# Kernel tuning notes

Measured on AMD Instinct MI355X. Metric: run time of the kernel, lower is better.

## Reference

```python
import jax, jax.numpy as jnp
import numpy as np
import math

B, M, N, K = 4, 8192, 8192, 16
FD = 64       # in_fdim == out_fdim (residual add)
HID = 128     # args.hidden_dim
G = 8         # args.ngroups


def index_points(points, idx):
    # points: (B, C, N), idx: (B, M, K) -> (B, C, M, K)
    return jax.vmap(lambda p, i: p[:, i])(points, idx)


def conv1d(x, w, b):  # 1x1 Conv1d: x (B,Ci,M), w (Co,Ci)
    return jnp.einsum('oi,bim->bom', w, x) + b[None, :, None]


def conv2d(x, w, b):  # 1x1 Conv2d: x (B,Ci,M,K), w (Co,Ci)
    return jnp.einsum('oi,bimk->bomk', w, x) + b[None, :, None, None]


def group_norm(x, w, b, eps=1e-5):
    # torch GroupNorm over (C//G, M, K) per group per sample
    Bb, C, Mm, Kk = x.shape
    xr = x.reshape(Bb, G, C // G, Mm, Kk)
    mu = xr.mean(axis=(2, 3, 4), keepdims=True)
    var = xr.var(axis=(2, 3, 4), keepdims=True)
    xr = (xr - mu) * jax.lax.rsqrt(var + eps)
    return xr.reshape(Bb, C, Mm, Kk) * w[None, :, None, None] + b[None, :, None, None]


def setup_inputs() -> dict:
    key = jax.random.key(0)
    ks = jax.random.split(key, 24)
    s = 0.05
    inp = {
        'q_xyzs': jax.random.normal(ks[0], (B, 3, M), jnp.float32),
        'k_xyzs': jax.random.normal(ks[1], (B, 3, N), jnp.float32),
        'q_feats': jax.random.normal(ks[2], (B, FD, M), jnp.float32),
        'k_feats': jax.random.normal(ks[3], (B, FD, N), jnp.float32),
        'v_feats': jax.random.normal(ks[4], (B, FD, N), jnp.float32),
        'knn_idx': jax.random.randint(ks[5], (B, M, K), 0, N),
        'mask': jnp.ones((B, M, K), dtype=bool),
        'wq_w': jax.random.normal(ks[6], (HID, FD)) * s, 'wq_b': jnp.zeros((HID,)),
        'wk_w': jax.random.normal(ks[7], (HID, FD)) * s, 'wk_b': jnp.zeros((HID,)),
        'wv_w': jax.random.normal(ks[8], (HID, FD)) * s, 'wv_b': jnp.zeros((HID,)),
        'd1_w': jax.random.normal(ks[9], (HID, 3)) * s, 'd1_b': jnp.zeros((HID,)),
        'dgn_w': jnp.ones((HID,)), 'dgn_b': jnp.zeros((HID,)),
        'd2_w': jax.random.normal(ks[10], (HID, HID)) * s, 'd2_b': jnp.zeros((HID,)),
        'g1_w': jax.random.normal(ks[11], (HID, HID)) * s, 'g1_b': jnp.zeros((HID,)),
        'ggn_w': jnp.ones((HID,)), 'ggn_b': jnp.zeros((HID,)),
        'g2_w': jax.random.normal(ks[12], (HID, HID)) * s, 'g2_b': jnp.zeros((HID,)),
        'post_w': jax.random.normal(ks[13], (FD, HID)) * s, 'post_b': jnp.zeros((FD,)),
    }
    return inp


def reference(q_xyzs, k_xyzs, q_feats, k_feats, v_feats, knn_idx, mask,
              wq_w, wq_b, wk_w, wk_b, wv_w, wv_b,
              d1_w, d1_b, dgn_w, dgn_b, d2_w, d2_b,
              g1_w, g1_b, ggn_w, ggn_b, g2_w, g2_b,
              post_w, post_b):
    knn_xyzs = index_points(k_xyzs, knn_idx)                 # (B,3,M,K)
    pre = q_feats
    query = conv1d(q_feats, wq_w, wq_b)                      # (B,HID,M)
    key = index_points(conv1d(k_feats, wk_w, wk_b), knn_idx) # (B,HID,M,K)
    value = index_points(conv1d(v_feats, wv_w, wv_b), knn_idx)

    rel = q_xyzs[:, :, :, None] - knn_xyzs                   # (B,3,M,K)
    pos_enc = conv2d(jax.nn.relu(group_norm(conv2d(rel, d1_w, d1_b), dgn_w, dgn_b)), d2_w, d2_b)

    attn_in = query[:, :, :, None] - key + pos_enc
    attn = conv2d(jax.nn.relu(group_norm(conv2d(attn_in, g1_w, g1_b), ggn_w, ggn_b)), g2_w, g2_b)
    attn = attn / math.sqrt(HID)
    attn = jnp.where(mask[:, None], attn, -jnp.finfo(attn.dtype).max)
    attn = jax.nn.softmax(attn, axis=-1)                     # over neighbor axis K

    res = jnp.einsum('bcmk,bcmk->bcm', attn, value + pos_enc)
    return conv1d(res, post_w, post_b) + pre
```

## Files before the change

### kernel.cpp

```cpp
#include <hip/hip_runtime.h>
#include <hip/hip_bf16.h>

typedef __attribute__((ext_vector_type(8))) short short8;
typedef __attribute__((ext_vector_type(4))) float f32x4;
typedef unsigned short ushort_t;

#define B_    4
#define M_    8192
#define N_    8192
#define KNN   16
#define FD    64
#define HID   128
#define CNT   (M_*KNN)
#define SCALE 0.08838834764831845f

#define QT_OFF       0ULL
#define KT_OFF       4194304ULL
#define VT_OFF       6291456ULL
#define WD2_OFF      8388608ULL
#define WFO_OFF      8396800ULL
#define WG2_OFF      8404992ULL
#define WQ2T_OFF     8413184ULL
#define WK2T_OFF     8421376ULL
#define WVT_OFF      8429568ULL
#define POSTT_OFF    8437760ULL
#define G2BS_OFF     8445952ULL
#define BQ_OFF       8446080ULL
#define BK_OFF       8446208ULL
#define HAFF_OFF     8446336ULL
#define RELSTATS_OFF 8448384ULL
#define YSUM_OFF     8448448ULL
#define YSQ_OFF      8448960ULL
#define GGNA_OFF     8449472ULL
#define GGNB_OFF     8449984ULL

__device__ __forceinline__ ushort_t f2bf(float x) {
    return (ushort_t)((__float_as_uint(x) + 0x8000u) >> 16);
}
__device__ __forceinline__ unsigned pk2bf(float a, float b) {
    unsigned ua = __float_as_uint(a) + 0x8000u;
    unsigned ub = __float_as_uint(b) + 0x8000u;
    return (ua >> 16) | (ub & 0xFFFF0000u);
}
__device__ __forceinline__ float bf2f(ushort_t b) {
    union { unsigned u; float f; } v; v.u = ((unsigned)b) << 16;
    return v.f;
}

__global__ __launch_bounds__(256) void k_prep(
    const float* __restrict__ d2, const float* __restrict__ g1, const float* __restrict__ g2,
    const float* __restrict__ wq, const float* __restrict__ wk, const float* __restrict__ wv,
    const float* __restrict__ post, const float* __restrict__ g2b,
    const float* __restrict__ wq_b, const float* __restrict__ wk_b,
    const float* __restrict__ d2b, const float* __restrict__ g1b,
    float* __restrict__ ws)
{
    int tid = blockIdx.x * 256 + threadIdx.x;
    if (tid < 16384) {
        int j = tid & 7, lane = (tid >> 3) & 63, s = (tid >> 9) & 3, ct = tid >> 11;
        int row = ct*16 + (lane & 15);
        int colk = s*32 + (lane >> 4)*8 + j;
        ((ushort_t*)(ws + WD2_OFF))[tid] = f2bf(d2[row*HID + colk]);
        ((ushort_t*)(ws + WG2_OFF))[tid] = f2bf(g2[row*HID + colk] * SCALE);
        float acc = 0.f;
        #pragma unroll 8
        for (int t = 0; t < HID; t++) acc += g1[row*HID + t] * d2[t*HID + colk];
        ((ushort_t*)(ws + WFO_OFF))[tid] = f2bf(acc);
    }
    if (tid < 8192) {
        int f = tid >> 7, j = tid & 127;
        ws[POSTT_OFF + j*64 + f] = post[tid];
        int i = tid >> 7, c = tid & 127;
        float aq = 0.f, ak = 0.f;
        #pragma unroll 8
        for (int h = 0; h < HID; h++) {
            float g = g1[c*HID + h];
            aq += g * wq[h*FD + i];
            ak += g * wk[h*FD + i];
        }
        ws[WQ2T_OFF + tid] = aq;
        ws[WK2T_OFF + tid] = ak;
        ws[WVT_OFF + tid] = wv[c*FD + i];
    }
    if (tid < 128) {
        ws[G2BS_OFF + tid] = g2b[tid] * SCALE;
        float bq = g1b[tid], bk = 0.f;
        #pragma unroll 8
        for (int h = 0; h < HID; h++) {
            float g = g1[tid*HID + h];
            bq += g * (wq_b[h] + d2b[h]);
            bk += g * wk_b[h];
        }
        ws[BQ_OFF + tid] = bq;
        ws[BK_OFF + tid] = bk;
    }
}

__global__ __launch_bounds__(256) void k_transform(
    const float* __restrict__ qf, const float* __restrict__ kf, const float* __restrict__ vf,
    const float* __restrict__ wv_b, float* __restrict__ ws)
{
    __shared__ __align__(16) float sF[64*36];
    int tid = threadIdx.x;
    int t = blockIdx.y;
    int gm0 = blockIdx.x * 32;
    int b = gm0 >> 13, m0 = gm0 & (M_-1);
    const float* in = (t==0) ? qf : (t==1) ? kf : vf;
    const float* wT = ws + ((t==0) ? WQ2T_OFF : (t==1) ? WK2T_OFF : WVT_OFF);
    {
        int i = tid >> 2, sg = tid & 3;
        const float* src = in + ((size_t)b*FD + i)*M_ + m0 + sg*8;
        *(f32x4*)&sF[i*36 + sg*8]     = *(const f32x4*)src;
        *(f32x4*)&sF[i*36 + sg*8 + 4] = *(const f32x4*)(src + 4);
    }
    __syncthreads();
    int c = tid & 127, h = tid >> 7;
    float bc = (t==0) ? ws[BQ_OFF + c] : (t==1) ? ws[BK_OFF + c] : wv_b[c];
    float acc[16];
    #pragma unroll
    for (int p = 0; p < 16; p++) acc[p] = bc;
    #pragma unroll 4
    for (int i = 0; i < 64; i++) {
        float w = wT[i*128 + c];
        #pragma unroll
        for (int pq = 0; pq < 4; pq++) {
            f32x4 fv = *(const f32x4*)&sF[i*36 + h*16 + pq*4];
            acc[pq*4+0] += w*fv[0]; acc[pq*4+1] += w*fv[1];
            acc[pq*4+2] += w*fv[2]; acc[pq*4+3] += w*fv[3];
        }
    }
    if (t == 0) {
        #pragma unroll
        for (int p = 0; p < 16; p++)
            ws[QT_OFF + (size_t)(gm0 + h*16 + p)*HID + c] = acc[p];
    } else {
        ushort_t* o = (ushort_t*)(ws + ((t==1) ? KT_OFF : VT_OFF));
        #pragma unroll
        for (int p = 0; p < 16; p++)
            o[(size_t)(gm0 + h*16 + p)*HID + c] = f2bf(acc[p]);
    }
}

__global__ __launch_bounds__(256) void k_relstats(
    const float* __restrict__ qx, const float* __restrict__ kx,
    const int* __restrict__ knn, float* __restrict__ ws)
{
    int tid = threadIdx.x;
    int b = blockIdx.y;
    int m = blockIdx.x * 256 + tid;
    const float* qb = qx + (size_t)b*3*M_;
    const float* kb = kx + (size_t)b*3*N_;
    const int* kn = knn + ((size_t)b*M_ + m)*KNN;
    float a[9] = {0,0,0,0,0,0,0,0,0};
    float q0 = qb[m], q1 = qb[M_+m], q2 = qb[2*M_+m];
    #pragma unroll
    for (int k = 0; k < KNN; k++) {
        int id = kn[k];
        float r0 = q0 - kb[id], r1 = q1 - kb[N_+id], r2 = q2 - kb[2*N_+id];
        a[0]+=r0; a[1]+=r1; a[2]+=r2;
        a[3]+=r0*r0; a[4]+=r0*r1; a[5]+=r0*r2;
        a[6]+=r1*r1; a[7]+=r1*r2; a[8]+=r2*r2;
    }
    __shared__ float red[4];
    float* rs = ws + RELSTATS_OFF + b*16;
    for (int q = 0; q < 9; q++) {
        float v = a[q];
        #pragma unroll
        for (int o = 32; o > 0; o >>= 1) v += __shfl_down(v, o, 64);
        if ((tid & 63) == 0) red[tid >> 6] = v;
        __syncthreads();
        if (tid == 0) atomicAdd(&rs[q], red[0]+red[1]+red[2]+red[3]);
        __syncthreads();
    }
}

__global__ __launch_bounds__(512) void k_dgn(
    const float* __restrict__ d1w, const float* __restrict__ d1b,
    const float* __restrict__ gw, const float* __restrict__ gb,
    float* __restrict__ ws)
{
    __shared__ float sm_[512], sq_[512], smu[32], srs[32];
    int t = threadIdx.x, b = t >> 7, c = t & 127;
    const float* rs = ws + RELSTATS_OFF + b*16;
    float inv = 1.0f / (float)CNT;
    float x0 = rs[0]*inv, x1 = rs[1]*inv, x2 = rs[2]*inv;
    float S00 = rs[3]*inv, S01 = rs[4]*inv, S02 = rs[5]*inv;
    float S11 = rs[6]*inv, S12 = rs[7]*inv, S22 = rs[8]*inv;
    float w0 = d1w[c*3], w1 = d1w[c*3+1], w2 = d1w[c*3+2], bc = d1b[c];
    float mc = w0*x0 + w1*x1 + w2*x2 + bc;
    float qc = w0*w0*S00 + w1*w1*S11 + w2*w2*S22
             + 2.f*(w0*w1*S01 + w0*w2*S02 + w1*w2*S12)
             + 2.f*bc*(mc - bc) + bc*bc;
    sm_[t] = mc; sq_[t] = qc;
    __syncthreads();
    if (t < 32) {
        int bb = t >> 3, g = t & 7;
        float mu = 0, ey = 0;
        for (int j = 0; j < 16; j++) { mu += sm_[bb*128 + g*16 + j]; ey += sq_[bb*128 + g*16 + j]; }
        mu *= (1.f/16.f); ey *= (1.f/16.f);
        smu[t] = mu; srs[t] = rsqrtf(ey - mu*mu + 1e-5f);
    }
    __syncthreads();
    int g = c >> 4;
    float al = gw[c] * srs[b*8 + g];
    float be = gb[c] - smu[b*8 + g] * al;
    f32x4 h; h[0] = al*w0; h[1] = al*w1; h[2] = al*w2; h[3] = al*bc + be;
    *(f32x4*)(ws + HAFF_OFF + ((size_t)b*128 + c)*4) = h;
}

__global__ __launch_bounds__(512) void k_ggn(
    const float* __restrict__ gw, const float* __restrict__ gb, float* __restrict__ ws)
{
    __shared__ float smu[32], srs[32];
    int t = threadIdx.x, b = t >> 7, c = t & 127;
    if (t < 32) {
        int bb = t >> 3, g = t & 7;
        float s1 = 0, s2 = 0;
        for (int j = 0; j < 16; j++) {
            s1 += ws[YSUM_OFF + bb*128 + g*16 + j];
            s2 += ws[YSQ_OFF  + bb*128 + g*16 + j];
        }
        float invn = 1.f / (16.f * (float)CNT);
        float mu = s1*invn, ey = s2*invn;
        smu[t] = mu; srs[t] = rsqrtf(ey - mu*mu + 1e-5f);
    }
    __syncthreads();
    int g = c >> 4;
    float al = gw[c] * srs[b*8 + g];
    float be = gb[c] - smu[b*8 + g] * al;
    ws[GGNA_OFF + b*128 + c] = al;
    ws[GGNB_OFF + b*128 + c] = be;
}

struct SmemPipe {
    union {
        ushort_t tP[4][16*136];
        struct { f32x4 haff[128]; float rel[4][16][4]; } pre;
    } u;
    ushort_t tH[4][16*136];
    float ga[128], gb[128];
    float res[4][128];
    int idx[64];
};

template<bool STATS>
__global__ __launch_bounds__(256, 4) void k_pipe(
    const float* __restrict__ qx, const float* __restrict__ kx, const int* __restrict__ knn,
    const float* __restrict__ qf, const float* __restrict__ d2b, const float* __restrict__ postb,
    float* __restrict__ ws, float* __restrict__ out)
{
    __shared__ SmemPipe sm;
    int tid = threadIdx.x, wid = tid >> 6, lane = tid & 63;
    int ln = lane & 15, q = lane >> 4;
    int gm0 = blockIdx.x * 4;
    int b = gm0 >> 13, m0 = gm0 & (M_-1);
    int ct0 = wid * 2;

    if (tid < 64) {
        int id = knn[(size_t)gm0*KNN + tid];
        sm.idx[tid] = id;
        int p = tid >> 4, nn = tid & 15;
        int m = m0 + p;
        sm.u.pre.rel[p][nn][0] = qx[(size_t)b*3*M_ + m]        - kx[(size_t)b*3*N_ + id];
        sm.u.pre.rel[p][nn][1] = qx[(size_t)b*3*M_ + M_ + m]   - kx[(size_t)b*3*N_ + N_ + id];
        sm.u.pre.rel[p][nn][2] = qx[(size_t)b*3*M_ + 2*M_ + m] - kx[(size_t)b*3*N_ + 2*N_ + id];
    }
    if (tid < 128) {
        sm.u.pre.haff[tid] = *(const f32x4*)(ws + HAFF_OFF + ((size_t)b*128 + tid)*4);
        if (STATS) { sm.ga[tid] = 0.f; sm.gb[tid] = 0.f; }
        else { sm.ga[tid] = ws[GGNA_OFF + b*128 + tid]; sm.gb[tid] = ws[GGNB_OFF + b*128 + tid]; }
    }
    __syncthreads();

    {
        int p = tid >> 6, n = (tid >> 2) & 15, cb = tid & 3;
        float r0 = sm.u.pre.rel[p][n][0];
        float r1 = sm.u.pre.rel[p][n][1];
        float r2 = sm.u.pre.rel[p][n][2];
        unsigned* dst = (unsigned*)&sm.tH[p][n*136 + cb*32];
        #pragma unroll
        for (int jj = 0; jj < 32; jj += 2) {
            f32x4 h1 = sm.u.pre.haff[cb*32 + jj];
            f32x4 h2 = sm.u.pre.haff[cb*32 + jj + 1];
            float a = fmaf(h1[0], r0, fmaf(h1[1], r1, fmaf(h1[2], r2, h1[3])));
            float c = fmaf(h2[0], r0, fmaf(h2[1], r1, fmaf(h2[2], r2, h2[3])));
            dst[jj >> 1] = pk2bf(a > 0.f ? a : 0.f, c > 0.f ? c : 0.f);
        }
    }
    __syncthreads();

    const short8* wd2 = (const short8*)(ws + WD2_OFF);
    const short8* wfo = (const short8*)(ws + WFO_OFF);
    const ushort_t* ktb = (const ushort_t*)(ws + KT_OFF);
    const ushort_t* vtb = (const ushort_t*)(ws + VT_OFF);

    f32x4 bid2[2], gav[2], gbv[2];
    if (!STATS) {
        #pragma unroll
        for (int cc = 0; cc < 2; cc++) {
            int row0 = (ct0+cc)*16 + q*4;
            bid2[cc] = *(const f32x4*)(d2b + row0);
            gav[cc] = *(const f32x4*)&sm.ga[row0];
            gbv[cc] = *(const f32x4*)&sm.gb[row0];
        }
    }
    float s1[2][4], s2[2][4];
    if (STATS) {
        #pragma unroll
        for (int cc = 0; cc < 2; cc++)
            #pragma unroll
            for (int r = 0; r < 4; r++) { s1[cc][r] = 0.f; s2[cc][r] = 0.f; }
    }

    for (int p = 0; p < 4; p++) {
        int gm = gm0 + p;
        short8 bh[4];
        #pragma unroll
        for (int s = 0; s < 4; s++)
            bh[s] = *(const short8*)&sm.tH[p][ln*136 + s*32 + q*8];

        f32x4 accY[2];
        #pragma unroll
        for (int cc = 0; cc < 2; cc++) {
            f32x4 a = {0.f,0.f,0.f,0.f};
            #pragma unroll
            for (int s = 0; s < 4; s++)
                a = __builtin_amdgcn_mfma_f32_16x16x32_bf16(wfo[((ct0+cc)*4+s)*64 + lane], bh[s], a, 0,0,0);
            accY[cc] = a;
        }
        if (!STATS) {
            #pragma unroll
            for (int cc = 0; cc < 2; cc++) {
                f32x4 a = {0.f,0.f,0.f,0.f};
                #pragma unroll
                for (int s = 0; s < 4; s++)
                    a = __builtin_amdgcn_mfma_f32_16x16x32_bf16(wd2[((ct0+cc)*4+s)*64 + lane], bh[s], a, 0,0,0);
                int row0 = (ct0+cc)*16 + q*4;
                uint2 pv;
                pv.x = pk2bf(a[0]+bid2[cc][0], a[1]+bid2[cc][1]);
                pv.y = pk2bf(a[2]+bid2[cc][2], a[3]+bid2[cc][3]);
                *(uint2*)&sm.u.tP[p][ln*136 + row0] = pv;
            }
        }
        int id = sm.idx[p*16 + ln];
        float yv[2][4];
        #pragma unroll
        for (int cc = 0; cc < 2; cc++) {
            int row0 = (ct0+cc)*16 + q*4;
            f32x4 qv = *(const f32x4*)(ws + QT_OFF + (size_t)gm*HID + row0);
            uint2 kv = *(const uint2*)(ktb + ((size_t)b*N_ + id)*HID + row0);
            yv[cc][0] = accY[cc][0] + qv[0] - bf2f((ushort_t)(kv.x & 0xffff));
            yv[cc][1] = accY[cc][1] + qv[1] - bf2f((ushort_t)(kv.x >> 16));
            yv[cc][2] = accY[cc][2] + qv[2] - bf2f((ushort_t)(kv.y & 0xffff));
            yv[cc][3] = accY[cc][3] + qv[3] - bf2f((ushort_t)(kv.y >> 16));
        }
        if (STATS) {
            #pragma unroll
            for (int cc = 0; cc < 2; cc++)
                #pragma unroll
                for (int r = 0; r < 4; r++) { s1[cc][r] += yv[cc][r]; s2[cc][r] += yv[cc][r]*yv[cc][r]; }
        } else {
            __syncthreads();
            #pragma unroll
            for (int cc = 0; cc < 2; cc++) {
                int row0 = (ct0+cc)*16 + q*4;
                float y0 = fmaf(gav[cc][0], yv[cc][0], gbv[cc][0]);
                float y1 = fmaf(gav[cc][1], yv[cc][1], gbv[cc][1]);
                float y2 = fmaf(gav[cc][2], yv[cc][2], gbv[cc][2]);
                float y3 = fmaf(gav[cc][3], yv[cc][3], gbv[cc][3]);
                uint2 yw;
                yw.x = pk2bf(y0 > 0.f ? y0 : 0.f, y1 > 0.f ? y1 : 0.f);
                yw.y = pk2bf(y2 > 0.f ? y2 : 0.f, y3 > 0.f ? y3 : 0.f);
                *(uint2*)&sm.tH[p][ln*136 + row0] = yw;
            }
        }
    }

    if (STATS) {
        #pragma unroll
        for (int cc = 0; cc < 2; cc++)
            #pragma unroll
            for (int r = 0; r < 4; r++) {
                float v1 = s1[cc][r], v2 = s2[cc][r];
                v1 += __shfl_xor(v1,1,64); v1 += __shfl_xor(v1,2,64);
                v1 += __shfl_xor(v1,4,64); v1 += __shfl_xor(v1,8,64);
                v2 += __shfl_xor(v2,1,64); v2 += __shfl_xor(v2,2,64);
                v2 += __shfl_xor(v2,4,64); v2 += __shfl_xor(v2,8,64);
                if (ln == 0) {
                    atomicAdd(&sm.ga[(ct0+cc)*16 + q*4 + r], v1);
                    atomicAdd(&sm.gb[(ct0+cc)*16 + q*4 + r], v2);
                }
            }
        __syncthreads();
        if (tid < 128) {
            atomicAdd(&ws[YSUM_OFF + b*128 + tid], sm.ga[tid]);
            atomicAdd(&ws[YSQ_OFF  + b*128 + tid], sm.gb[tid]);
        }
        return;
    }

    {
        int p = tid >> 6, n = (tid >> 2) & 15, cb = tid & 3;
        int id = sm.idx[p*16 + n];
        const ushort_t* vr = vtb + ((size_t)b*N_ + id)*HID + cb*32;
        ushort_t* pr = &sm.u.tP[p][n*136 + cb*32];
        #pragma unroll
        for (int u = 0; u < 4; u++) {
            short8 vv = *(const short8*)(vr + u*8);
            short8 pp = *(const short8*)(pr + u*8);
            unsigned w[4];
            #pragma unroll
            for (int j = 0; j < 4; j++) {
                float a = bf2f((ushort_t)vv[j*2])   + bf2f((ushort_t)pp[j*2]);
                float c = bf2f((ushort_t)vv[j*2+1]) + bf2f((ushort_t)pp[j*2+1]);
                w[j] = pk2bf(a, c);
            }
            *(short8*)(pr + u*8) = *(short8*)w;
        }
    }
    __syncthreads();

    {
        const short8* wg2 = (const short8*)(ws + WG2_OFF);
        #pragma unroll
        for (int p = 0; p < 4; p++) {
            short8 ay[4];
            #pragma unroll
            for (int s = 0; s < 4; s++)
                ay[s] = *(const short8*)&sm.tH[p][ln*136 + s*32 + q*8];
            #pragma unroll
            for (int cc = 0; cc < 2; cc++) {
                int cout = (ct0+cc)*16 + ln;
                f32x4 a = {0.f,0.f,0.f,0.f};
                #pragma unroll
                for (int s = 0; s < 4; s++)
                    a = __builtin_amdgcn_mfma_f32_16x16x32_bf16(ay[s], wg2[((ct0+cc)*4+s)*64 + lane], a, 0,0,0);
                float zb = ws[G2BS_OFF + cout];
                float den = 0.f, num = 0.f;
                #pragma unroll
                for (int r = 0; r < 4; r++) {
                    float e = __expf(a[r] + zb);
                    den += e;
                    num += e * bf2f(sm.u.tP[p][(q*4+r)*136 + cout]);
                }
                den += __shfl_xor(den, 16, 64); den += __shfl_xor(den, 32, 64);
                num += __shfl_xor(num, 16, 64); num += __shfl_xor(num, 32, 64);
                if (q == 0) sm.res[p][cout] = num / den;
            }
        }
    }
    __syncthreads();

    {
        int f = tid >> 2, p = tid & 3;
        const float* pt = ws + POSTT_OFF;
        const float* rr = sm.res[p];
        float acc = postb[f];
        #pragma unroll 8
        for (int j = 0; j < 128; j++) acc += pt[j*64 + f] * rr[j];
        size_t o = (size_t)b*FD*M_ + (size_t)f*M_ + m0 + p;
        out[o] = acc + qf[o];
    }
}

extern "C" void kernel_launch(void* const* d_in, const int* in_sizes, int n_in,
                              void* d_out, int out_size, void* d_ws, size_t ws_size,
                              hipStream_t stream)
{
    const float* q_xyzs = (const float*)d_in[0];
    const float* k_xyzs = (const float*)d_in[1];
    const float* q_feats= (const float*)d_in[2];
    const float* k_feats= (const float*)d_in[3];
    const float* v_feats= (const float*)d_in[4];
    const int*   knn    = (const int*)d_in[5];
    const float* wq_w = (const float*)d_in[7];  const float* wq_b = (const float*)d_in[8];
    const float* wk_w = (const float*)d_in[9];  const float* wk_b = (const float*)d_in[10];
    const float* wv_w = (const float*)d_in[11]; const float* wv_b = (const float*)d_in[12];
    const float* d1_w = (const float*)d_in[13]; const float* d1_b = (const float*)d_in[14];
    const float* dgn_w= (const float*)d_in[15]; const float* dgn_b= (const float*)d_in[16];
    const float* d2_w = (const float*)d_in[17]; const float* d2_b = (const float*)d_in[18];
    const float* g1_w = (const float*)d_in[19]; const float* g1_b = (const float*)d_in[20];
    const float* ggn_w= (const float*)d_in[21]; const float* ggn_b= (const float*)d_in[22];
    const float* g2_w = (const float*)d_in[23]; const float* g2_b = (const float*)d_in[24];
    const float* post_w=(const float*)d_in[25]; const float* post_b=(const float*)d_in[26];
    float* ws  = (float*)d_ws;
    float* out = (float*)d_out;

    hipMemsetAsync(ws + RELSTATS_OFF, 0, 1088*sizeof(float), stream);

    k_prep<<<64, 256, 0, stream>>>(d2_w, g1_w, g2_w, wq_w, wk_w, wv_w,
                                   post_w, g2_b, wq_b, wk_b, d2_b, g1_b, ws);
    k_transform<<<dim3(B_*M_/32, 3), 256, 0, stream>>>(q_feats, k_feats, v_feats, wv_b, ws);
    k_relstats<<<dim3(M_/256, B_), 256, 0, stream>>>(q_xyzs, k_xyzs, knn, ws);
    k_dgn<<<1, 512, 0, stream>>>(d1_w, d1_b, dgn_w, dgn_b, ws);
    k_pipe<true><<<B_*M_/4, 256, 0, stream>>>(
        q_xyzs, k_xyzs, knn, q_feats, d2_b, post_b, ws, out);
    k_ggn<<<1, 512, 0, stream>>>(ggn_w, ggn_b, ws);
    k_pipe<false><<<B_*M_/4, 256, 0, stream>>>(
        q_xyzs, k_xyzs, knn, q_feats, d2_b, post_b, ws, out);
}
```

Before: 527.0 us.

## Cache pre-norm attention activations between passes and stage output through transpose kernel

The stats pass now writes the pre-GroupNorm activations to the workspace as bf16 when enough workspace is available. The second pass reloads them instead of recomputing the first MFMA product and the key gather. Key gathers are issued early to hide latency, and the rel-projection loop is rotated to reduce LDS bank conflicts. The final output is staged in the workspace and transposed by a new k_out kernel for coalesced stores. This trades extra HBM traffic (about 64MB written and read) for less recompute and gather work, plus one extra launch.

```diff
diff --git a/kernel.cpp b/kernel.cpp
--- a/kernel.cpp
+++ b/kernel.cpp
@@ -33,6 +33,9 @@
 #define YSQ_OFF      8448960ULL
 #define GGNA_OFF     8449472ULL
 #define GGNB_OFF     8449984ULL
+#define OUTS_OFF     8450496ULL
+#define YW_OFF       10547648ULL
+#define WS_NEED_BIG  ((10547648ULL + 16777216ULL) * 4ULL)
 
 __device__ __forceinline__ ushort_t f2bf(float x) {
     return (ushort_t)((__float_as_uint(x) + 0x8000u) >> 16);
@@ -243,11 +246,11 @@
     int idx[64];
 };
 
-template<bool STATS>
+template<bool STATS, bool STOREY, bool LOADY>
 __global__ __launch_bounds__(256, 4) void k_pipe(
     const float* __restrict__ qx, const float* __restrict__ kx, const int* __restrict__ knn,
-    const float* __restrict__ qf, const float* __restrict__ d2b, const float* __restrict__ postb,
-    float* __restrict__ ws, float* __restrict__ out)
+    const float* __restrict__ d2b, const float* __restrict__ postb,
+    float* __restrict__ ws)
 {
     __shared__ SmemPipe sm;
     int tid = threadIdx.x, wid = tid >> 6, lane = tid & 63;
@@ -272,38 +275,43 @@
     }
     __syncthreads();
 
+    const ushort_t* ktb = (const ushort_t*)(ws + KT_OFF);
+    const ushort_t* vtb = (const ushort_t*)(ws + VT_OFF);
+
+    uint2 kvp[4][2];
+    if (!LOADY) {
+        #pragma unroll
+        for (int p = 0; p < 4; p++) {
+            int id = sm.idx[p*16 + ln];
+            const ushort_t* kr = ktb + ((size_t)b*N_ + id)*HID;
+            #pragma unroll
+            for (int cc = 0; cc < 2; cc++)
+                kvp[p][cc] = *(const uint2*)(kr + (ct0+cc)*16 + q*4);
+        }
+    }
+
     {
         int p = tid >> 6, n = (tid >> 2) & 15, cb = tid & 3;
         float r0 = sm.u.pre.rel[p][n][0];
         float r1 = sm.u.pre.rel[p][n][1];
         float r2 = sm.u.pre.rel[p][n][2];
         unsigned* dst = (unsigned*)&sm.tH[p][n*136 + cb*32];
-        #pragma unroll
-        for (int jj = 0; jj < 32; jj += 2) {
-            f32x4 h1 = sm.u.pre.haff[cb*32 + jj];
-            f32x4 h2 = sm.u.pre.haff[cb*32 + jj + 1];
+        int rot = ((((n >> 3) & 1) | (((cb >> 1) & 1) << 1)) << 2);
+        #pragma unroll
+        for (int t = 0; t < 16; t++) {
+            int o = (t + rot) & 15;
+            f32x4 h1 = sm.u.pre.haff[cb*32 + 2*o];
+            f32x4 h2 = sm.u.pre.haff[cb*32 + 2*o + 1];
             float a = fmaf(h1[0], r0, fmaf(h1[1], r1, fmaf(h1[2], r2, h1[3])));
             float c = fmaf(h2[0], r0, fmaf(h2[1], r1, fmaf(h2[2], r2, h2[3])));
-            dst[jj >> 1] = pk2bf(a > 0.f ? a : 0.f, c > 0.f ? c : 0.f);
-        }
-    }
-    __syncthreads();
-
+            dst[o] = pk2bf(a > 0.f ? a : 0.f, c > 0.f ? c : 0.f);
+        }
+    }
+    __syncthreads();
+
+    const short8* wfo = (const short8*)(ws + WFO_OFF);
     const short8* wd2 = (const short8*)(ws + WD2_OFF);
-    const short8* wfo = (const short8*)(ws + WFO_OFF);
-    const ushort_t* ktb = (const ushort_t*)(ws + KT_OFF);
-    const ushort_t* vtb = (const ushort_t*)(ws + VT_OFF);
-
-    f32x4 bid2[2], gav[2], gbv[2];
-    if (!STATS) {
-        #pragma unroll
-        for (int cc = 0; cc < 2; cc++) {
-            int row0 = (ct0+cc)*16 + q*4;
-            bid2[cc] = *(const f32x4*)(d2b + row0);
-            gav[cc] = *(const f32x4*)&sm.ga[row0];
-            gbv[cc] = *(const f32x4*)&sm.gb[row0];
-        }
-    }
+
     float s1[2][4], s2[2][4];
     if (STATS) {
         #pragma unroll
@@ -311,7 +319,19 @@
             #pragma unroll
             for (int r = 0; r < 4; r++) { s1[cc][r] = 0.f; s2[cc][r] = 0.f; }
     }
-
+    uint2 yp[4][2];
+    f32x4 bid2[2], ga_[2], gb_[2];
+    #pragma unroll
+    for (int cc = 0; cc < 2; cc++) {
+        int row0 = (ct0+cc)*16 + q*4;
+        if (!STATS) {
+            bid2[cc] = *(const f32x4*)(d2b + row0);
+            ga_[cc] = *(const f32x4*)&sm.ga[row0];
+            gb_[cc] = *(const f32x4*)&sm.gb[row0];
+        }
+    }
+
+    #pragma unroll
     for (int p = 0; p < 4; p++) {
         int gm = gm0 + p;
         short8 bh[4];
@@ -319,14 +339,33 @@
         for (int s = 0; s < 4; s++)
             bh[s] = *(const short8*)&sm.tH[p][ln*136 + s*32 + q*8];
 
-        f32x4 accY[2];
-        #pragma unroll
-        for (int cc = 0; cc < 2; cc++) {
-            f32x4 a = {0.f,0.f,0.f,0.f};
-            #pragma unroll
-            for (int s = 0; s < 4; s++)
-                a = __builtin_amdgcn_mfma_f32_16x16x32_bf16(wfo[((ct0+cc)*4+s)*64 + lane], bh[s], a, 0,0,0);
-            accY[cc] = a;
+        if (!LOADY) {
+            #pragma unroll
+            for (int cc = 0; cc < 2; cc++) {
+                int row0 = (ct0+cc)*16 + q*4;
+                f32x4 a = {0.f,0.f,0.f,0.f};
+                #pragma unroll
+                for (int s = 0; s < 4; s++)
+                    a = __builtin_amdgcn_mfma_f32_16x16x32_bf16(wfo[((ct0+cc)*4+s)*64 + lane], bh[s], a, 0,0,0);
+                f32x4 qv = *(const f32x4*)(ws + QT_OFF + (size_t)gm*HID + row0);
+                uint2 kv = kvp[p][cc];
+                float y0 = a[0] + qv[0] - bf2f((ushort_t)(kv.x & 0xffff));
+                float y1 = a[1] + qv[1] - bf2f((ushort_t)(kv.x >> 16));
+                float y2 = a[2] + qv[2] - bf2f((ushort_t)(kv.y & 0xffff));
+                float y3 = a[3] + qv[3] - bf2f((ushort_t)(kv.y >> 16));
+                if (STATS) {
+                    s1[cc][0]+=y0; s1[cc][1]+=y1; s1[cc][2]+=y2; s1[cc][3]+=y3;
+                    s2[cc][0]+=y0*y0; s2[cc][1]+=y1*y1; s2[cc][2]+=y2*y2; s2[cc][3]+=y3*y3;
+                    if (STOREY) { yp[p][cc].x = pk2bf(y0,y1); yp[p][cc].y = pk2bf(y2,y3); }
+                } else {
+                    float t0 = fmaf(ga_[cc][0], y0, gb_[cc][0]);
+                    float t1 = fmaf(ga_[cc][1], y1, gb_[cc][1]);
+                    float t2 = fmaf(ga_[cc][2], y2, gb_[cc][2]);
+                    float t3 = fmaf(ga_[cc][3], y3, gb_[cc][3]);
+                    yp[p][cc].x = pk2bf(t0 > 0.f ? t0 : 0.f, t1 > 0.f ? t1 : 0.f);
+                    yp[p][cc].y = pk2bf(t2 > 0.f ? t2 : 0.f, t3 > 0.f ? t3 : 0.f);
+                }
+            }
         }
         if (!STATS) {
             #pragma unroll
@@ -342,41 +381,26 @@
                 *(uint2*)&sm.u.tP[p][ln*136 + row0] = pv;
             }
         }
-        int id = sm.idx[p*16 + ln];
-        float yv[2][4];
-        #pragma unroll
-        for (int cc = 0; cc < 2; cc++) {
-            int row0 = (ct0+cc)*16 + q*4;
-            f32x4 qv = *(const f32x4*)(ws + QT_OFF + (size_t)gm*HID + row0);
-            uint2 kv = *(const uint2*)(ktb + ((size_t)b*N_ + id)*HID + row0);
-            yv[cc][0] = accY[cc][0] + qv[0] - bf2f((ushort_t)(kv.x & 0xffff));
-            yv[cc][1] = accY[cc][1] + qv[1] - bf2f((ushort_t)(kv.x >> 16));
-            yv[cc][2] = accY[cc][2] + qv[2] - bf2f((ushort_t)(kv.y & 0xffff));
-            yv[cc][3] = accY[cc][3] + qv[3] - bf2f((ushort_t)(kv.y >> 16));
-        }
-        if (STATS) {
-            #pragma unroll
-            for (int cc = 0; cc < 2; cc++)
+    }
+
+    if (STATS) {
+        if (STOREY) {
+            __syncthreads();
+            #pragma unroll
+            for (int p = 0; p < 4; p++)
                 #pragma unroll
-                for (int r = 0; r < 4; r++) { s1[cc][r] += yv[cc][r]; s2[cc][r] += yv[cc][r]*yv[cc][r]; }
-        } else {
+                for (int cc = 0; cc < 2; cc++)
+                    *(uint2*)&sm.tH[p][ln*136 + (ct0+cc)*16 + q*4] = yp[p][cc];
             __syncthreads();
-            #pragma unroll
-            for (int cc = 0; cc < 2; cc++) {
-                int row0 = (ct0+cc)*16 + q*4;
-                float y0 = fmaf(gav[cc][0], yv[cc][0], gbv[cc][0]);
-                float y1 = fmaf(gav[cc][1], yv[cc][1], gbv[cc][1]);
-                float y2 = fmaf(gav[cc][2], yv[cc][2], gbv[cc][2]);
-                float y3 = fmaf(gav[cc][3], yv[cc][3], gbv[cc][3]);
-                uint2 yw;
-                yw.x = pk2bf(y0 > 0.f ? y0 : 0.f, y1 > 0.f ? y1 : 0.f);
-                yw.y = pk2bf(y2 > 0.f ? y2 : 0.f, y3 > 0.f ? y3 : 0.f);
-                *(uint2*)&sm.tH[p][ln*136 + row0] = yw;
-            }
-        }
-    }
-
-    if (STATS) {
+            {
+                int p = tid >> 6, n = (tid >> 2) & 15, cb = tid & 3;
+                ushort_t* yw = (ushort_t*)(ws + YW_OFF);
+                const short8* src = (const short8*)&sm.tH[p][n*136 + cb*32];
+                short8* dst = (short8*)(yw + ((size_t)(gm0+p)*16 + n)*HID + cb*32);
+                #pragma unroll
+                for (int u = 0; u < 4; u++) dst[u] = src[u];
+            }
+        }
         #pragma unroll
         for (int cc = 0; cc < 2; cc++)
             #pragma unroll
@@ -399,6 +423,36 @@
         return;
     }
 
+    __syncthreads();
+
+    if (LOADY) {
+        int p = tid >> 6, n = (tid >> 2) & 15, cb = tid & 3;
+        const ushort_t* yw = (const ushort_t*)(ws + YW_OFF);
+        const short8* src = (const short8*)(yw + ((size_t)(gm0+p)*16 + n)*HID + cb*32);
+        ushort_t* dst = &sm.tH[p][n*136 + cb*32];
+        #pragma unroll
+        for (int u = 0; u < 4; u++) {
+            short8 yv8 = src[u];
+            f32x4 a0 = *(const f32x4*)&sm.ga[cb*32 + u*8];
+            f32x4 a1 = *(const f32x4*)&sm.ga[cb*32 + u*8 + 4];
+            f32x4 b0 = *(const f32x4*)&sm.gb[cb*32 + u*8];
+            f32x4 b1 = *(const f32x4*)&sm.gb[cb*32 + u*8 + 4];
+            unsigned w[4];
+            #pragma unroll
+            for (int j = 0; j < 4; j++) {
+                float ya = fmaf((j<2?a0:a1)[(j*2)&3],   bf2f((ushort_t)yv8[j*2]),   (j<2?b0:b1)[(j*2)&3]);
+                float yb = fmaf((j<2?a0:a1)[(j*2+1)&3], bf2f((ushort_t)yv8[j*2+1]), (j<2?b0:b1)[(j*2+1)&3]);
+                w[j] = pk2bf(ya > 0.f ? ya : 0.f, yb > 0.f ? yb : 0.f);
+            }
+            *(short8*)(dst + u*8) = *(short8*)w;
+        }
+    } else {
+        #pragma unroll
+        for (int p = 0; p < 4; p++)
+            #pragma unroll
+            for (int cc = 0; cc < 2; cc++)
+                *(uint2*)&sm.tH[p][ln*136 + (ct0+cc)*16 + q*4] = yp[p][cc];
+    }
     {
         int p = tid >> 6, n = (tid >> 2) & 15, cb = tid & 3;
         int id = sm.idx[p*16 + n];
@@ -458,8 +512,29 @@
         float acc = postb[f];
         #pragma unroll 8
         for (int j = 0; j < 128; j++) acc += pt[j*64 + f] * rr[j];
-        size_t o = (size_t)b*FD*M_ + (size_t)f*M_ + m0 + p;
-        out[o] = acc + qf[o];
+        ws[OUTS_OFF + (size_t)(gm0 + p)*FD + f] = acc;
+    }
+}
+
+__global__ __launch_bounds__(256) void k_out(
+    const float* __restrict__ qf, const float* __restrict__ ws, float* __restrict__ out)
+{
+    __shared__ float sT[64][65];
+    int tid = threadIdx.x;
+    int b = blockIdx.y, m0 = blockIdx.x * 64;
+    const float* stg = ws + OUTS_OFF + ((size_t)b*M_ + m0)*FD;
+    #pragma unroll
+    for (int it = 0; it < 16; it++) {
+        int idx = it*256 + tid;
+        sT[idx >> 6][idx & 63] = stg[idx];
+    }
+    __syncthreads();
+    #pragma unroll
+    for (int it = 0; it < 16; it++) {
+        int idx = it*256 + tid;
+        int f = idx >> 6, mm = idx & 63;
+        size_t o = (size_t)b*FD*M_ + (size_t)f*M_ + m0 + mm;
+        out[o] = sT[mm][f] + qf[o];
     }
 }
 
@@ -486,6 +561,8 @@
     float* ws  = (float*)d_ws;
     float* out = (float*)d_out;
 
+    bool big = (ws_size >= WS_NEED_BIG);
+
     hipMemsetAsync(ws + RELSTATS_OFF, 0, 1088*sizeof(float), stream);
 
     k_prep<<<64, 256, 0, stream>>>(d2_w, g1_w, g2_w, wq_w, wk_w, wv_w,
@@ -493,9 +570,14 @@
     k_transform<<<dim3(B_*M_/32, 3), 256, 0, stream>>>(q_feats, k_feats, v_feats, wv_b, ws);
     k_relstats<<<dim3(M_/256, B_), 256, 0, stream>>>(q_xyzs, k_xyzs, knn, ws);
     k_dgn<<<1, 512, 0, stream>>>(d1_w, d1_b, dgn_w, dgn_b, ws);
-    k_pipe<true><<<B_*M_/4, 256, 0, stream>>>(
-        q_xyzs, k_xyzs, knn, q_feats, d2_b, post_b, ws, out);
+    if (big)
+        k_pipe<true, true, false><<<B_*M_/4, 256, 0, stream>>>(q_xyzs, k_xyzs, knn, d2_b, post_b, ws);
+    else
+        k_pipe<true, false, false><<<B_*M_/4, 256, 0, stream>>>(q_xyzs, k_xyzs, knn, d2_b, post_b, ws);
     k_ggn<<<1, 512, 0, stream>>>(ggn_w, ggn_b, ws);
-    k_pipe<false><<<B_*M_/4, 256, 0, stream>>>(
-        q_xyzs, k_xyzs, knn, q_feats, d2_b, post_b, ws, out);
-}
+    if (big)
+        k_pipe<false, false, true><<<B_*M_/4, 256, 0, stream>>>(q_xyzs, k_xyzs, knn, d2_b, post_b, ws);
+    else
+        k_pipe<false, false, false><<<B_*M_/4, 256, 0, stream>>>(q_xyzs, k_xyzs, knn, d2_b, post_b, ws);
+    k_out<<<dim3(M_/64, B_), 256, 0, stream>>>(q_feats, ws, out);
+}
```

Measured after the change: 488.4 us. 7.3% less time.

## Materialize pre-norm attention activations in stats pass and reuse in main pass

Applied to the files above, without the earlier changes.

The stats pass now writes the pre-GroupNorm attention activations (bf16, fragment layout) to workspace, and the main pass reloads them instead of recomputing the fused MFMA and re-gathering key rows. Key xyz coordinates are repacked into a float4-per-point table so each neighbour gather is one vector load. The query projection is stored as bf16, and the haff loop is rotated per thread to spread LDS bank access. The trade is an extra 64 MB write and read of intermediates in exchange for fewer gathers and MFMAs in the main kernel.

```diff
diff --git a/kernel.cpp b/kernel.cpp
--- a/kernel.cpp
+++ b/kernel.cpp
@@ -15,24 +15,27 @@
 #define SCALE 0.08838834764831845f
 
 #define QT_OFF       0ULL
-#define KT_OFF       4194304ULL
-#define VT_OFF       6291456ULL
-#define WD2_OFF      8388608ULL
-#define WFO_OFF      8396800ULL
-#define WG2_OFF      8404992ULL
-#define WQ2T_OFF     8413184ULL
-#define WK2T_OFF     8421376ULL
-#define WVT_OFF      8429568ULL
-#define POSTT_OFF    8437760ULL
-#define G2BS_OFF     8445952ULL
-#define BQ_OFF       8446080ULL
-#define BK_OFF       8446208ULL
-#define HAFF_OFF     8446336ULL
-#define RELSTATS_OFF 8448384ULL
-#define YSUM_OFF     8448448ULL
-#define YSQ_OFF      8448960ULL
-#define GGNA_OFF     8449472ULL
-#define GGNB_OFF     8449984ULL
+#define KT_OFF       2097152ULL
+#define VT_OFF       4194304ULL
+#define WD2_OFF      6291456ULL
+#define WFO_OFF      6299648ULL
+#define WG2_OFF      6307840ULL
+#define WQ2T_OFF     6316032ULL
+#define WK2T_OFF     6324224ULL
+#define WVT_OFF      6332416ULL
+#define POSTT_OFF    6340608ULL
+#define G2BS_OFF     6348800ULL
+#define BQ_OFF       6348928ULL
+#define BK_OFF       6349056ULL
+#define HAFF_OFF     6349184ULL
+#define RELSTATS_OFF 6351232ULL
+#define YSUM_OFF     6351296ULL
+#define YSQ_OFF      6351808ULL
+#define GGNA_OFF     6352320ULL
+#define GGNB_OFF     6352832ULL
+#define KXI_OFF      6353344ULL
+#define YW_OFF       6484416ULL
+#define WS_NEED_YW   ((YW_OFF + 33554432ULL) * 4ULL)
 
 __device__ __forceinline__ ushort_t f2bf(float x) {
     return (ushort_t)((__float_as_uint(x) + 0x8000u) >> 16);
@@ -53,7 +56,7 @@
     const float* __restrict__ post, const float* __restrict__ g2b,
     const float* __restrict__ wq_b, const float* __restrict__ wk_b,
     const float* __restrict__ d2b, const float* __restrict__ g1b,
-    float* __restrict__ ws)
+    const float* __restrict__ kx, float* __restrict__ ws)
 {
     int tid = blockIdx.x * 256 + threadIdx.x;
     if (tid < 16384) {
@@ -82,6 +85,19 @@
         ws[WK2T_OFF + tid] = ak;
         ws[WVT_OFF + tid] = wv[c*FD + i];
     }
+    #pragma unroll
+    for (int r = 0; r < 2; r++) {
+        int i = tid*2 + r;
+        if (i < B_*N_) {
+            int bb = i >> 13, id = i & (N_-1);
+            f32x4 v;
+            v[0] = kx[(size_t)bb*3*N_ + id];
+            v[1] = kx[(size_t)bb*3*N_ + N_ + id];
+            v[2] = kx[(size_t)bb*3*N_ + 2*N_ + id];
+            v[3] = 0.f;
+            *(f32x4*)(ws + KXI_OFF + (size_t)i*4) = v;
+        }
+    }
     if (tid < 128) {
         ws[G2BS_OFF + tid] = g2b[tid] * SCALE;
         float bq = g1b[tid], bk = 0.f;
@@ -129,34 +145,27 @@
             acc[pq*4+2] += w*fv[2]; acc[pq*4+3] += w*fv[3];
         }
     }
-    if (t == 0) {
-        #pragma unroll
-        for (int p = 0; p < 16; p++)
-            ws[QT_OFF + (size_t)(gm0 + h*16 + p)*HID + c] = acc[p];
-    } else {
-        ushort_t* o = (ushort_t*)(ws + ((t==1) ? KT_OFF : VT_OFF));
-        #pragma unroll
-        for (int p = 0; p < 16; p++)
-            o[(size_t)(gm0 + h*16 + p)*HID + c] = f2bf(acc[p]);
-    }
+    ushort_t* o = (ushort_t*)(ws + ((t==0) ? QT_OFF : (t==1) ? KT_OFF : VT_OFF));
+    #pragma unroll
+    for (int p = 0; p < 16; p++)
+        o[(size_t)(gm0 + h*16 + p)*HID + c] = f2bf(acc[p]);
 }
 
 __global__ __launch_bounds__(256) void k_relstats(
-    const float* __restrict__ qx, const float* __restrict__ kx,
-    const int* __restrict__ knn, float* __restrict__ ws)
+    const float* __restrict__ qx, const int* __restrict__ knn, float* __restrict__ ws)
 {
     int tid = threadIdx.x;
     int b = blockIdx.y;
     int m = blockIdx.x * 256 + tid;
     const float* qb = qx + (size_t)b*3*M_;
-    const float* kb = kx + (size_t)b*3*N_;
+    const f32x4* kxi = (const f32x4*)(ws + KXI_OFF) + (size_t)b*N_;
     const int* kn = knn + ((size_t)b*M_ + m)*KNN;
     float a[9] = {0,0,0,0,0,0,0,0,0};
     float q0 = qb[m], q1 = qb[M_+m], q2 = qb[2*M_+m];
     #pragma unroll
     for (int k = 0; k < KNN; k++) {
-        int id = kn[k];
-        float r0 = q0 - kb[id], r1 = q1 - kb[N_+id], r2 = q2 - kb[2*N_+id];
+        f32x4 kc = kxi[kn[k]];
+        float r0 = q0 - kc[0], r1 = q1 - kc[1], r2 = q2 - kc[2];
         a[0]+=r0; a[1]+=r1; a[2]+=r2;
         a[3]+=r0*r0; a[4]+=r0*r1; a[5]+=r0*r2;
         a[6]+=r1*r1; a[7]+=r1*r2; a[8]+=r2*r2;
@@ -232,7 +241,128 @@
     ws[GGNB_OFF + b*128 + c] = be;
 }
 
-struct SmemPipe {
+struct SmemS {
+    f32x4 haff[128];
+    float rel[4][16][4];
+    int idx[64];
+    ushort_t tH[4][16*136];
+    ushort_t tK[4][16*136];
+    float ga[128], gb[128];
+};
+
+__global__ __launch_bounds__(256, 4) void k_stats(
+    const float* __restrict__ qx, const int* __restrict__ knn, float* __restrict__ ws)
+{
+    __shared__ SmemS sm;
+    int tid = threadIdx.x, wid = tid >> 6, lane = tid & 63;
+    int ln = lane & 15, q = lane >> 4;
+    int gm0 = blockIdx.x * 4;
+    int b = gm0 >> 13, m0 = gm0 & (M_-1);
+    int ct0 = wid * 2;
+
+    if (tid < 64) {
+        int id = knn[(size_t)gm0*KNN + tid];
+        sm.idx[tid] = id;
+        int p = tid >> 4, nn = tid & 15;
+        int m = m0 + p;
+        f32x4 kc = *(const f32x4*)(ws + KXI_OFF + ((size_t)b*N_ + id)*4);
+        sm.rel[p][nn][0] = qx[(size_t)b*3*M_ + m]        - kc[0];
+        sm.rel[p][nn][1] = qx[(size_t)b*3*M_ + M_ + m]   - kc[1];
+        sm.rel[p][nn][2] = qx[(size_t)b*3*M_ + 2*M_ + m] - kc[2];
+    }
+    if (tid < 128) {
+        sm.haff[tid] = *(const f32x4*)(ws + HAFF_OFF + ((size_t)b*128 + tid)*4);
+        sm.ga[tid] = 0.f; sm.gb[tid] = 0.f;
+    }
+    __syncthreads();
+
+    const ushort_t* qtb = (const ushort_t*)(ws + QT_OFF);
+    const ushort_t* ktb = (const ushort_t*)(ws + KT_OFF);
+
+    {
+        int p = tid >> 6, n = (tid >> 2) & 15, cb = tid & 3;
+        int id = sm.idx[p*16 + n];
+        const short8* kr = (const short8*)(ktb + ((size_t)b*N_ + id)*HID + cb*32);
+        short8 kld0 = kr[0], kld1 = kr[1], kld2 = kr[2], kld3 = kr[3];
+
+        float r0 = sm.rel[p][n][0];
+        float r1 = sm.rel[p][n][1];
+        float r2 = sm.rel[p][n][2];
+        unsigned* dst = (unsigned*)&sm.tH[p][n*136 + cb*32];
+        int rot = ((((n >> 3) & 1) | (((cb >> 1) & 1) << 1)) << 2);
+        #pragma unroll
+        for (int t = 0; t < 16; t++) {
+            int o = (t + rot) & 15;
+            f32x4 h1 = sm.haff[cb*32 + 2*o];
+            f32x4 h2 = sm.haff[cb*32 + 2*o + 1];
+            float a = fmaf(h1[0], r0, fmaf(h1[1], r1, fmaf(h1[2], r2, h1[3])));
+            float c = fmaf(h2[0], r0, fmaf(h2[1], r1, fmaf(h2[2], r2, h2[3])));
+            dst[o] = pk2bf(a > 0.f ? a : 0.f, c > 0.f ? c : 0.f);
+        }
+        short8* kdst = (short8*)&sm.tK[p][n*136 + cb*32];
+        kdst[0] = kld0; kdst[1] = kld1; kdst[2] = kld2; kdst[3] = kld3;
+    }
+    __syncthreads();
+
+    const short8* wfo = (const short8*)(ws + WFO_OFF);
+    uint2* yw8 = (uint2*)(ws + YW_OFF);
+
+    float s1[2][4], s2[2][4];
+    #pragma unroll
+    for (int cc = 0; cc < 2; cc++)
+        #pragma unroll
+        for (int r = 0; r < 4; r++) { s1[cc][r] = 0.f; s2[cc][r] = 0.f; }
+
+    #pragma unroll
+    for (int p = 0; p < 4; p++) {
+        int gm = gm0 + p;
+        short8 bh[4];
+        #pragma unroll
+        for (int s = 0; s < 4; s++)
+            bh[s] = *(const short8*)&sm.tH[p][ln*136 + s*32 + q*8];
+
+        #pragma unroll
+        for (int cc = 0; cc < 2; cc++) {
+            f32x4 a = {0.f,0.f,0.f,0.f};
+            #pragma unroll
+            for (int s = 0; s < 4; s++)
+                a = __builtin_amdgcn_mfma_f32_16x16x32_bf16(wfo[((ct0+cc)*4+s)*64 + lane], bh[s], a, 0,0,0);
+            int row0 = (ct0+cc)*16 + q*4;
+            uint2 qv = *(const uint2*)(qtb + (size_t)gm*HID + row0);
+            uint2 kv = *(const uint2*)&sm.tK[p][ln*136 + row0];
+            float y0 = a[0] + bf2f((ushort_t)(qv.x & 0xffff)) - bf2f((ushort_t)(kv.x & 0xffff));
+            float y1 = a[1] + bf2f((ushort_t)(qv.x >> 16))    - bf2f((ushort_t)(kv.x >> 16));
+            float y2 = a[2] + bf2f((ushort_t)(qv.y & 0xffff)) - bf2f((ushort_t)(kv.y & 0xffff));
+            float y3 = a[3] + bf2f((ushort_t)(qv.y >> 16))    - bf2f((ushort_t)(kv.y >> 16));
+            s1[cc][0]+=y0; s1[cc][1]+=y1; s1[cc][2]+=y2; s1[cc][3]+=y3;
+            s2[cc][0]+=y0*y0; s2[cc][1]+=y1*y1; s2[cc][2]+=y2*y2; s2[cc][3]+=y3*y3;
+            uint2 yv; yv.x = pk2bf(y0,y1); yv.y = pk2bf(y2,y3);
+            yw8[((size_t)gm*8 + ct0+cc)*64 + lane] = yv;
+        }
+    }
+
+    #pragma unroll
+    for (int cc = 0; cc < 2; cc++)
+        #pragma unroll
+        for (int r = 0; r < 4; r++) {
+            float v1 = s1[cc][r], v2 = s2[cc][r];
+            v1 += __shfl_xor(v1,1,64); v1 += __shfl_xor(v1,2,64);
+            v1 += __shfl_xor(v1,4,64); v1 += __shfl_xor(v1,8,64);
+            v2 += __shfl_xor(v2,1,64); v2 += __shfl_xor(v2,2,64);
+            v2 += __shfl_xor(v2,4,64); v2 += __shfl_xor(v2,8,64);
+            if (ln == 0) {
+                atomicAdd(&sm.ga[(ct0+cc)*16 + q*4 + r], v1);
+                atomicAdd(&sm.gb[(ct0+cc)*16 + q*4 + r], v2);
+            }
+        }
+    __syncthreads();
+    if (tid < 128) {
+        atomicAdd(&ws[YSUM_OFF + b*128 + tid], sm.ga[tid]);
+        atomicAdd(&ws[YSQ_OFF  + b*128 + tid], sm.gb[tid]);
+    }
+}
+
+struct SmemM {
     union {
         ushort_t tP[4][16*136];
         struct { f32x4 haff[128]; float rel[4][16][4]; } pre;
@@ -243,34 +373,46 @@
     int idx[64];
 };
 
-template<bool STATS>
-__global__ __launch_bounds__(256, 4) void k_pipe(
-    const float* __restrict__ qx, const float* __restrict__ kx, const int* __restrict__ knn,
-    const float* __restrict__ qf, const float* __restrict__ d2b, const float* __restrict__ postb,
-    float* __restrict__ ws, float* __restrict__ out)
-{
-    __shared__ SmemPipe sm;
+__global__ __launch_bounds__(256, 4) void k_main(
+    const float* __restrict__ qx, const int* __restrict__ knn,
+    const float* __restrict__ d2b, const float* __restrict__ postb,
+    const float* __restrict__ qf, float* __restrict__ ws, float* __restrict__ out)
+{
+    __shared__ SmemM sm;
     int tid = threadIdx.x, wid = tid >> 6, lane = tid & 63;
     int ln = lane & 15, q = lane >> 4;
     int gm0 = blockIdx.x * 4;
     int b = gm0 >> 13, m0 = gm0 & (M_-1);
     int ct0 = wid * 2;
 
+    uint2 ywp[4][2];
+    {
+        const uint2* yw8 = (const uint2*)(ws + YW_OFF);
+        #pragma unroll
+        for (int p = 0; p < 4; p++)
+            #pragma unroll
+            for (int cc = 0; cc < 2; cc++)
+                ywp[p][cc] = yw8[((size_t)(gm0+p)*8 + ct0+cc)*64 + lane];
+    }
+
     if (tid < 64) {
         int id = knn[(size_t)gm0*KNN + tid];
         sm.idx[tid] = id;
         int p = tid >> 4, nn = tid & 15;
         int m = m0 + p;
-        sm.u.pre.rel[p][nn][0] = qx[(size_t)b*3*M_ + m]        - kx[(size_t)b*3*N_ + id];
-        sm.u.pre.rel[p][nn][1] = qx[(size_t)b*3*M_ + M_ + m]   - kx[(size_t)b*3*N_ + N_ + id];
-        sm.u.pre.rel[p][nn][2] = qx[(size_t)b*3*M_ + 2*M_ + m] - kx[(size_t)b*3*N_ + 2*N_ + id];
+        f32x4 kc = *(const f32x4*)(ws + KXI_OFF + ((size_t)b*N_ + id)*4);
+        sm.u.pre.rel[p][nn][0] = qx[(size_t)b*3*M_ + m]        - kc[0];
+        sm.u.pre.rel[p][nn][1] = qx[(size_t)b*3*M_ + M_ + m]   - kc[1];
+        sm.u.pre.rel[p][nn][2] = qx[(size_t)b*3*M_ + 2*M_ + m] - kc[2];
     }
     if (tid < 128) {
         sm.u.pre.haff[tid] = *(const f32x4*)(ws + HAFF_OFF + ((size_t)b*128 + tid)*4);
-        if (STATS) { sm.ga[tid] = 0.f; sm.gb[tid] = 0.f; }
-        else { sm.ga[tid] = ws[GGNA_OFF + b*128 + tid]; sm.gb[tid] = ws[GGNB_OFF + b*128 + tid]; }
-    }
-    __syncthreads();
+        sm.ga[tid] = ws[GGNA_OFF + b*128 + tid];
+        sm.gb[tid] = ws[GGNB_OFF + b*128 + tid];
+    }
+    __syncthreads();
+
+    const ushort_t* vtb = (const ushort_t*)(ws + VT_OFF);
 
     {
         int p = tid >> 6, n = (tid >> 2) & 15, cb = tid & 3;
@@ -278,127 +420,65 @@
         float r1 = sm.u.pre.rel[p][n][1];
         float r2 = sm.u.pre.rel[p][n][2];
         unsigned* dst = (unsigned*)&sm.tH[p][n*136 + cb*32];
-        #pragma unroll
-        for (int jj = 0; jj < 32; jj += 2) {
-            f32x4 h1 = sm.u.pre.haff[cb*32 + jj];
-            f32x4 h2 = sm.u.pre.haff[cb*32 + jj + 1];
+        int rot = ((((n >> 3) & 1) | (((cb >> 1) & 1) << 1)) << 2);
+        #pragma unroll
+        for (int t = 0; t < 16; t++) {
+            int o = (t + rot) & 15;
+            f32x4 h1 = sm.u.pre.haff[cb*32 + 2*o];
+            f32x4 h2 = sm.u.pre.haff[cb*32 + 2*o + 1];
             float a = fmaf(h1[0], r0, fmaf(h1[1], r1, fmaf(h1[2], r2, h1[3])));
             float c = fmaf(h2[0], r0, fmaf(h2[1], r1, fmaf(h2[2], r2, h2[3])));
-            dst[jj >> 1] = pk2bf(a > 0.f ? a : 0.f, c > 0.f ? c : 0.f);
+            dst[o] = pk2bf(a > 0.f ? a : 0.f, c > 0.f ? c : 0.f);
         }
     }
     __syncthreads();
 
     const short8* wd2 = (const short8*)(ws + WD2_OFF);
-    const short8* wfo = (const short8*)(ws + WFO_OFF);
-    const ushort_t* ktb = (const ushort_t*)(ws + KT_OFF);
-    const ushort_t* vtb = (const ushort_t*)(ws + VT_OFF);
-
-    f32x4 bid2[2], gav[2], gbv[2];
-    if (!STATS) {
-        #pragma unroll
-        for (int cc = 0; cc < 2; cc++) {
-            int row0 = (ct0+cc)*16 + q*4;
-            bid2[cc] = *(const f32x4*)(d2b + row0);
-            gav[cc] = *(const f32x4*)&sm.ga[row0];
-            gbv[cc] = *(const f32x4*)&sm.gb[row0];
-        }
-    }
-    float s1[2][4], s2[2][4];
-    if (STATS) {
-        #pragma unroll
-        for (int cc = 0; cc < 2; cc++)
-            #pragma unroll
-            for (int r = 0; r < 4; r++) { s1[cc][r] = 0.f; s2[cc][r] = 0.f; }
-    }
-
+    f32x4 bid2[2], ga_[2], gb_[2];
+    #pragma unroll
+    for (int cc = 0; cc < 2; cc++) {
+        int row0 = (ct0+cc)*16 + q*4;
+        bid2[cc] = *(const f32x4*)(d2b + row0);
+        ga_[cc] = *(const f32x4*)&sm.ga[row0];
+        gb_[cc] = *(const f32x4*)&sm.gb[row0];
+    }
+
+    #pragma unroll
     for (int p = 0; p < 4; p++) {
-        int gm = gm0 + p;
         short8 bh[4];
         #pragma unroll
         for (int s = 0; s < 4; s++)
             bh[s] = *(const short8*)&sm.tH[p][ln*136 + s*32 + q*8];
-
-        f32x4 accY[2];
         #pragma unroll
         for (int cc = 0; cc < 2; cc++) {
             f32x4 a = {0.f,0.f,0.f,0.f};
             #pragma unroll
             for (int s = 0; s < 4; s++)
-                a = __builtin_amdgcn_mfma_f32_16x16x32_bf16(wfo[((ct0+cc)*4+s)*64 + lane], bh[s], a, 0,0,0);
-            accY[cc] = a;
-        }
-        if (!STATS) {
-            #pragma unroll
-            for (int cc = 0; cc < 2; cc++) {
-                f32x4 a = {0.f,0.f,0.f,0.f};
-                #pragma unroll
-                for (int s = 0; s < 4; s++)
-                    a = __builtin_amdgcn_mfma_f32_16x16x32_bf16(wd2[((ct0+cc)*4+s)*64 + lane], bh[s], a, 0,0,0);
-                int row0 = (ct0+cc)*16 + q*4;
-                uint2 pv;
-                pv.x = pk2bf(a[0]+bid2[cc][0], a[1]+bid2[cc][1]);
-                pv.y = pk2bf(a[2]+bid2[cc][2], a[3]+bid2[cc][3]);
-                *(uint2*)&sm.u.tP[p][ln*136 + row0] = pv;
-            }
-        }
-        int id = sm.idx[p*16 + ln];
-        float yv[2][4];
+                a = __builtin_amdgcn_mfma_f32_16x16x32_bf16(wd2[((ct0+cc)*4+s)*64 + lane], bh[s], a, 0,0,0);
+            int row0 = (ct0+cc)*16 + q*4;
+            uint2 pv;
+            pv.x = pk2bf(a[0]+bid2[cc][0], a[1]+bid2[cc][1]);
+            pv.y = pk2bf(a[2]+bid2[cc][2], a[3]+bid2[cc][3]);
+            *(uint2*)&sm.u.tP[p][ln*136 + row0] = pv;
+        }
+    }
+    __syncthreads();
+
+    #pragma unroll
+    for (int p = 0; p < 4; p++)
         #pragma unroll
         for (int cc = 0; cc < 2; cc++) {
             int row0 = (ct0+cc)*16 + q*4;
-            f32x4 qv = *(const f32x4*)(ws + QT_OFF + (size_t)gm*HID + row0);
-            uint2 kv = *(const uint2*)(ktb + ((size_t)b*N_ + id)*HID + row0);
-            yv[cc][0] = accY[cc][0] + qv[0] - bf2f((ushort_t)(kv.x & 0xffff));
-            yv[cc][1] = accY[cc][1] + qv[1] - bf2f((ushort_t)(kv.x >> 16));
-            yv[cc][2] = accY[cc][2] + qv[2] - bf2f((ushort_t)(kv.y & 0xffff));
-            yv[cc][3] = accY[cc][3] + qv[3] - bf2f((ushort_t)(kv.y >> 16));
-        }
-        if (STATS) {
-            #pragma unroll
-            for (int cc = 0; cc < 2; cc++)
-                #pragma unroll
-                for (int r = 0; r < 4; r++) { s1[cc][r] += yv[cc][r]; s2[cc][r] += yv[cc][r]*yv[cc][r]; }
-        } else {
-            __syncthreads();
-            #pragma unroll
-            for (int cc = 0; cc < 2; cc++) {
-                int row0 = (ct0+cc)*16 + q*4;
-                float y0 = fmaf(gav[cc][0], yv[cc][0], gbv[cc][0]);
-                float y1 = fmaf(gav[cc][1], yv[cc][1], gbv[cc][1]);
-                float y2 = fmaf(gav[cc][2], yv[cc][2], gbv[cc][2]);
-                float y3 = fmaf(gav[cc][3], yv[cc][3], gbv[cc][3]);
-                uint2 yw;
-                yw.x = pk2bf(y0 > 0.f ? y0 : 0.f, y1 > 0.f ? y1 : 0.f);
-                yw.y = pk2bf(y2 > 0.f ? y2 : 0.f, y3 > 0.f ? y3 : 0.f);
-                *(uint2*)&sm.tH[p][ln*136 + row0] = yw;
-            }
-        }
-    }
-
-    if (STATS) {
-        #pragma unroll
-        for (int cc = 0; cc < 2; cc++)
-            #pragma unroll
-            for (int r = 0; r < 4; r++) {
-                float v1 = s1[cc][r], v2 = s2[cc][r];
-                v1 += __shfl_xor(v1,1,64); v1 += __shfl_xor(v1,2,64);
-                v1 += __shfl_xor(v1,4,64); v1 += __shfl_xor(v1,8,64);
-                v2 += __shfl_xor(v2,1,64); v2 += __shfl_xor(v2,2,64);
-                v2 += __shfl_xor(v2,4,64); v2 += __shfl_xor(v2,8,64);
-                if (ln == 0) {
-                    atomicAdd(&sm.ga[(ct0+cc)*16 + q*4 + r], v1);
-                    atomicAdd(&sm.gb[(ct0+cc)*16 + q*4 + r], v2);
-                }
-            }
-        __syncthreads();
-        if (tid < 128) {
-            atomicAdd(&ws[YSUM_OFF + b*128 + tid], sm.ga[tid]);
-            atomicAdd(&ws[YSQ_OFF  + b*128 + tid], sm.gb[tid]);
-        }
-        return;
-    }
-
+            uint2 yv = ywp[p][cc];
+            float t0 = fmaf(ga_[cc][0], bf2f((ushort_t)(yv.x & 0xffff)), gb_[cc][0]);
+            float t1 = fmaf(ga_[cc][1], bf2f((ushort_t)(yv.x >> 16)),    gb_[cc][1]);
+            float t2 = fmaf(ga_[cc][2], bf2f((ushort_t)(yv.y & 0xffff)), gb_[cc][2]);
+            float t3 = fmaf(ga_[cc][3], bf2f((ushort_t)(yv.y >> 16)),    gb_[cc][3]);
+            uint2 yq2;
+            yq2.x = pk2bf(t0 > 0.f ? t0 : 0.f, t1 > 0.f ? t1 : 0.f);
+            yq2.y = pk2bf(t2 > 0.f ? t2 : 0.f, t3 > 0.f ? t3 : 0.f);
+            *(uint2*)&sm.tH[p][ln*136 + row0] = yq2;
+        }
     {
         int p = tid >> 6, n = (tid >> 2) & 15, cb = tid & 3;
         int id = sm.idx[p*16 + n];
@@ -489,13 +569,11 @@
     hipMemsetAsync(ws + RELSTATS_OFF, 0, 1088*sizeof(float), stream);
 
     k_prep<<<64, 256, 0, stream>>>(d2_w, g1_w, g2_w, wq_w, wk_w, wv_w,
-                                   post_w, g2_b, wq_b, wk_b, d2_b, g1_b, ws);
+                                   post_w, g2_b, wq_b, wk_b, d2_b, g1_b, k_xyzs, ws);
     k_transform<<<dim3(B_*M_/32, 3), 256, 0, stream>>>(q_feats, k_feats, v_feats, wv_b, ws);
-    k_relstats<<<dim3(M_/256, B_), 256, 0, stream>>>(q_xyzs, k_xyzs, knn, ws);
+    k_relstats<<<dim3(M_/256, B_), 256, 0, stream>>>(q_xyzs, knn, ws);
     k_dgn<<<1, 512, 0, stream>>>(d1_w, d1_b, dgn_w, dgn_b, ws);
-    k_pipe<true><<<B_*M_/4, 256, 0, stream>>>(
-        q_xyzs, k_xyzs, knn, q_feats, d2_b, post_b, ws, out);
+    k_stats<<<B_*M_/4, 256, 0, stream>>>(q_xyzs, knn, ws);
     k_ggn<<<1, 512, 0, stream>>>(ggn_w, ggn_b, ws);
-    k_pipe<false><<<B_*M_/4, 256, 0, stream>>>(
-        q_xyzs, k_xyzs, knn, q_feats, d2_b, post_b, ws, out);
-}
+    k_main<<<B_*M_/4, 256, 0, stream>>>(q_xyzs, knn, d2_b, post_b, q_feats, ws, out);
+}
```

New measurement: 528.7 us. No clear change (+0.3%).
